# Kernel tuning notes

Measured on AMD Instinct MI355X. Metric: run time of the kernel, lower is better.

## Reference

```python
import math
import jax, jax.numpy as jnp
import numpy as np

B, N = 1, 768
C_S, C_Z, C_H, H, PQ, PV = 384, 128, 16, 12, 4, 8
INF, EPS = 1e5, 1e-8
SOFTPLUS_INV_1 = 0.541324854612918


def setup_inputs() -> dict:
    key = jax.random.key(0)
    ks = jax.random.split(key, 20)
    p = lambda k, shape: (0.02 * jax.random.normal(k, shape)).astype(jnp.float32)
    hc = H * C_H
    inp = {
        's': jax.random.normal(ks[0], (B, N, C_S), dtype=jnp.float32),
        'z': jax.random.normal(ks[1], (B, N, N, C_Z), dtype=jnp.float32),
        'rot': jax.random.normal(ks[2], (B, N, 3, 3), dtype=jnp.float32),
        'trans': jax.random.normal(ks[3], (B, N, 3), dtype=jnp.float32),
        'mask': jnp.ones((B, N), dtype=jnp.float32),
        'w_q': p(ks[4], (hc, C_S)), 'b_q': p(ks[5], (hc,)),
        'w_kv': p(ks[6], (2 * hc, C_S)), 'b_kv': p(ks[7], (2 * hc,)),
        'w_qp': p(ks[8], (H * PQ * 3, C_S)), 'b_qp': p(ks[9], (H * PQ * 3,)),
        'w_kvp': p(ks[10], (H * (PQ + PV) * 3, C_S)), 'b_kvp': p(ks[11], (H * (PQ + PV) * 3,)),
        'w_b': p(ks[12], (H, C_Z)), 'b_b': p(ks[13], (H,)),
        'head_weights': jnp.full((H,), SOFTPLUS_INV_1, dtype=jnp.float32),
        'w_out': p(ks[14], (C_S, H * (C_Z + C_H + PV * 4))), 'b_out': p(ks[15], (C_S,)),
    }
    return inp


def reference(s, z, rot, trans, mask, w_q, b_q, w_kv, b_kv, w_qp, b_qp,
              w_kvp, b_kvp, w_b, b_b, head_weights, w_out, b_out):
    b_, n_ = s.shape[0], s.shape[1]
    # input projections
    q = (s @ w_q.T + b_q).reshape(b_, n_, H, C_H)              # [B,N,H,C]
    kv = (s @ w_kv.T + b_kv).reshape(b_, n_, H, 2 * C_H)
    k, v = kv[..., :C_H], kv[..., C_H:]
    bmat = z @ w_b.T + b_b                                      # [B,N,N,H]

    def make_pts(w, bias, P):
        x = s @ w.T + bias                                      # [B,N,3*H*P]
        # torch: split into 3 chunks of H*P, stack on last dim -> [B,N,H*P,3]
        x = x.reshape(b_, n_, 3, H * P).swapaxes(-1, -2)
        # rigid apply: R x + t (per residue)
        x = jnp.einsum('bnij,bnpj->bnpi', rot, x) + trans[:, :, None, :]
        return x.reshape(b_, n_, H, P, 3)

    q_pts = make_pts(w_qp, b_qp, PQ)                            # [B,N,H,PQ,3]
    kv_pts = make_pts(w_kvp, b_kvp, PQ + PV)
    k_pts, v_pts = kv_pts[..., :PQ, :], kv_pts[..., PQ:, :]     # [B,N,H,PQ/PV,3]

    # scalar QK attention
    a = jnp.einsum('bnhc,bmhc->bhnm', q, k) * math.sqrt(1.0 / (3 * C_H))
    a = a + math.sqrt(1.0 / 3) * jnp.moveaxis(bmat, -1, -3)     # pair bias

    # point-distance attention
    diff = q_pts[:, :, None] - k_pts[:, None]                   # [B,N,M,H,PQ,3]
    pt_att = jnp.sum(diff * diff, axis=-1)                      # [B,N,M,H,PQ]
    hw = jax.nn.softplus(head_weights) * math.sqrt(1.0 / (3 * (PQ * 9.0 / 2)))
    pt_att = -0.5 * jnp.sum(pt_att * hw[:, None], axis=-1)      # [B,N,M,H]
    a = a + jnp.moveaxis(pt_att, -1, -3)                        # [B,H,N,M]

    sq_mask = (mask[:, :, None] * mask[:, None, :] - 1.0) * INF
    a = jax.nn.softmax(a + sq_mask[:, None], axis=-1)           # [B,H,N,M]

    # outputs
    o = jnp.einsum('bhnm,bmhc->bnhc', a, v).reshape(b_, n_, H * C_H)
    o_pt = jnp.einsum('bhnm,bmhpc->bnhpc', a, v_pts)            # [B,N,H,PV,3]
    # rigid invert-apply: R^T (x - t)
    o_pt = jnp.einsum('bnji,bnhpj->bnhpi', rot, o_pt - trans[:, :, None, None, :])
    o_pt_norm = jnp.sqrt(jnp.sum(o_pt ** 2, axis=-1) + EPS).reshape(b_, n_, H * PV)
    o_pt = o_pt.reshape(b_, n_, H * PV, 3)
    o_pair = jnp.einsum('bhnm,bnmc->bnhc', a, z).reshape(b_, n_, H * C_Z)

    o_cat = jnp.concatenate(
        [o, o_pt[..., 0], o_pt[..., 1], o_pt[..., 2], o_pt_norm, o_pair], axis=-1)
    return o_cat @ w_out.T + b_out                              # [B,N,c_s]
```

## Files before the change

### kernel.cpp

```cpp
#include <hip/hip_runtime.h>

#define N_ 768
#define CS 384
#define CZ 128
#define HH 12
#define PQ_ 4
#define PV_ 8

__global__ __launch_bounds__(256, 4) void k_zb(
    const float* __restrict__ z,
    const float* __restrict__ w_b, const float* __restrict__ b_b,
    float* __restrict__ zbT)
{
    const int bid = blockIdx.x;
    const int n  = bid / 12;
    const int m0 = (bid % 12) * 64;
    const int tid = threadIdx.x;

    __shared__ float zs[64 * 133];
    __shared__ float zbt[64 * 13];

    const float4* zsrc = (const float4*)(z + ((size_t)n * N_ + m0) * CZ);
    #pragma unroll
    for (int j = 0; j < 8; ++j) {
        int idx = tid + j * 256;
        float4 zv = zsrc[idx];
        int f  = idx << 2;
        int ml = f >> 7;
        int c  = f & 127;
        float* d = &zs[ml * 133 + c];
        d[0] = zv.x; d[1] = zv.y; d[2] = zv.z; d[3] = zv.w;
    }
    __syncthreads();

    const int ml = tid & 63;
    const int hq = __builtin_amdgcn_readfirstlane(tid >> 6);
    const float* w0 = w_b + (hq * 3 + 0) * CZ;
    const float* w1 = w0 + CZ;
    const float* w2 = w1 + CZ;
    const float* zrow = &zs[ml * 133];
    float a0 = 0.f, a1 = 0.f, a2 = 0.f;
    #pragma unroll 8
    for (int c = 0; c < CZ; ++c) {
        float zv = zrow[c];
        a0 += zv * w0[c];
        a1 += zv * w1[c];
        a2 += zv * w2[c];
    }
    const float s3 = 0.5773502691896258f;
    zbt[ml * 13 + hq * 3 + 0] = s3 * (a0 + b_b[hq * 3 + 0]);
    zbt[ml * 13 + hq * 3 + 1] = s3 * (a1 + b_b[hq * 3 + 1]);
    zbt[ml * 13 + hq * 3 + 2] = s3 * (a2 + b_b[hq * 3 + 2]);
    __syncthreads();

    for (int idx = tid; idx < 768; idx += 256) {
        int h = idx >> 6, mm = idx & 63;
        zbT[(size_t)n * (HH * N_) + h * N_ + m0 + mm] = zbt[mm * 13 + h];
    }
}

__global__ __launch_bounds__(256, 4) void k_proj(
    const float* __restrict__ s,
    const float* __restrict__ rot,
    const float* __restrict__ trans,
    const float* __restrict__ w_q,  const float* __restrict__ b_q,
    const float* __restrict__ w_kv, const float* __restrict__ b_kv,
    const float* __restrict__ w_qp, const float* __restrict__ b_qp,
    const float* __restrict__ w_kvp,const float* __restrict__ b_kvp,
    float* __restrict__ q, float* __restrict__ kT,
    float* __restrict__ qp, float* __restrict__ kpT,
    float* __restrict__ vcat)
{
    const int rt = blockIdx.x % 48;
    const int nt = blockIdx.x / 48;
    const int r0 = rt * 24;
    const int n0 = nt * 64;
    const int tid = threadIdx.x;

    __shared__ float Ws[64][36];
    __shared__ float Ss[64][66];
    __shared__ float Rsh[64][9], Tsh[64][3];
    __shared__ float bsh[24];

    auto vmap = [&](int rv, const float*& wrow, float& bias) {
        if (rv < 192)      { wrow = w_q + (size_t)rv * CS;  bias = b_q[rv]; }
        else if (rv < 576) { int r = rv - 192; wrow = w_kv + (size_t)r * CS; bias = b_kv[r]; }
        else if (rv < 720) { int t = rv - 576; int hp = t / 3, d = t % 3;
                             int r = d * 48 + hp;  wrow = w_qp + (size_t)r * CS;  bias = b_qp[r]; }
        else               { int t = rv - 720; int j = t / 3, d = t % 3;
                             int r = d * 144 + j; wrow = w_kvp + (size_t)r * CS; bias = b_kvp[r]; }
    };

    if (tid < 24) {
        const float* wr; float bb;
        vmap(r0 + tid, wr, bb);
        bsh[tid] = bb;
    }
    if (r0 >= 576) {
        for (int idx = tid; idx < 64 * 9; idx += 256)
            Rsh[idx / 9][idx % 9] = rot[(size_t)(n0 + idx / 9) * 9 + idx % 9];
        for (int idx = tid; idx < 64 * 3; idx += 256)
            Tsh[idx / 3][idx % 3] = trans[(size_t)(n0 + idx / 3) * 3 + idx % 3];
    }

    const int g_n = tid & 31;
    const int g_r = tid >> 5;
    float acc[3][2] = {{0.f,0.f},{0.f,0.f},{0.f,0.f}};

    for (int ks = 0; ks < 6; ++ks) {
        const int kb = ks * 64;
        for (int t4 = tid; t4 < 384; t4 += 256) {
            int rl = t4 >> 4, c4 = t4 & 15;
            const float* wrow; float bb;
            vmap(r0 + rl, wrow, bb);
            float4 wv = *(const float4*)(wrow + kb + c4 * 4);
            int slot = (rl / 3) * 4 + rl % 3;
            Ws[c4 * 4 + 0][slot] = wv.x;
            Ws[c4 * 4 + 1][slot] = wv.y;
            Ws[c4 * 4 + 2][slot] = wv.z;
            Ws[c4 * 4 + 3][slot] = wv.w;
        }
        for (int t4 = tid; t4 < 1024; t4 += 256) {
            int nl = t4 >> 4, c4 = t4 & 15;
            float4 sv = *(const float4*)(s + (size_t)(n0 + nl) * CS + kb + c4 * 4);
            Ss[c4 * 4 + 0][nl] = sv.x;
            Ss[c4 * 4 + 1][nl] = sv.y;
            Ss[c4 * 4 + 2][nl] = sv.z;
            Ss[c4 * 4 + 3][nl] = sv.w;
        }
        __syncthreads();
        #pragma unroll 8
        for (int k = 0; k < 64; ++k) {
            float4 w  = *(const float4*)&Ws[k][g_r * 4];
            float2 sv = *(const float2*)&Ss[k][g_n * 2];
            acc[0][0] += w.x * sv.x;  acc[0][1] += w.x * sv.y;
            acc[1][0] += w.y * sv.x;  acc[1][1] += w.y * sv.y;
            acc[2][0] += w.z * sv.x;  acc[2][1] += w.z * sv.y;
        }
        __syncthreads();
    }

    const float b0 = bsh[g_r * 3 + 0];
    const float b1 = bsh[g_r * 3 + 1];
    const float b2 = bsh[g_r * 3 + 2];
    const int rvb = r0 + g_r * 3;

    if (rvb < 192) {
        #pragma unroll
        for (int nn = 0; nn < 2; ++nn) {
            int n = n0 + g_n * 2 + nn;
            q[(size_t)n * 192 + rvb + 0] = acc[0][nn] + b0;
            q[(size_t)n * 192 + rvb + 1] = acc[1][nn] + b1;
            q[(size_t)n * 192 + rvb + 2] = acc[2][nn] + b2;
        }
    } else if (rvb < 576) {
        #pragma unroll
        for (int cc = 0; cc < 3; ++cc) {
            int i = rvb + cc - 192;
            int h = i >> 5, c = i & 31;
            float bb = (cc == 0) ? b0 : (cc == 1) ? b1 : b2;
            if (c < 16) {
                float2 st = make_float2(acc[cc][0] + bb, acc[cc][1] + bb);
                *(float2*)&kT[(size_t)(h * 16 + c) * N_ + n0 + g_n * 2] = st;
            } else {
                vcat[(size_t)(n0 + g_n * 2 + 0) * 480 + h * 16 + c - 16] = acc[cc][0] + bb;
                vcat[(size_t)(n0 + g_n * 2 + 1) * 480 + h * 16 + c - 16] = acc[cc][1] + bb;
            }
        }
    } else if (rvb < 720) {
        int hp = (rvb - 576) / 3;
        #pragma unroll
        for (int nn = 0; nn < 2; ++nn) {
            int nl = g_n * 2 + nn, n = n0 + nl;
            float x = acc[0][nn] + b0, y = acc[1][nn] + b1, zc = acc[2][nn] + b2;
            const float* R = Rsh[nl];
            const float* T = Tsh[nl];
            #pragma unroll
            for (int d = 0; d < 3; ++d)
                qp[(size_t)n * 144 + hp * 3 + d] =
                    R[d * 3 + 0] * x + R[d * 3 + 1] * y + R[d * 3 + 2] * zc + T[d];
        }
    } else {
        int j = (rvb - 720) / 3;
        int h = j / 12, p = j % 12;
        float px[2][3];
        #pragma unroll
        for (int nn = 0; nn < 2; ++nn) {
            int nl = g_n * 2 + nn;
            float x = acc[0][nn] + b0, y = acc[1][nn] + b1, zc = acc[2][nn] + b2;
            const float* R = Rsh[nl];
            const float* T = Tsh[nl];
            #pragma unroll
            for (int d = 0; d < 3; ++d)
                px[nn][d] = R[d * 3 + 0] * x + R[d * 3 + 1] * y + R[d * 3 + 2] * zc + T[d];
        }
        if (p < PQ_) {
            #pragma unroll
            for (int d = 0; d < 3; ++d)
                *(float2*)&kpT[(size_t)(h * 12 + p * 3 + d) * N_ + n0 + g_n * 2] =
                    make_float2(px[0][d], px[1][d]);
        } else {
            int base = 192 + (h * PV_ + p - PQ_) * 3;
            #pragma unroll
            for (int nn = 0; nn < 2; ++nn) {
                int n = n0 + g_n * 2 + nn;
                #pragma unroll
                for (int d = 0; d < 3; ++d)
                    vcat[(size_t)n * 480 + base + d] = px[nn][d];
            }
        }
    }
}

__global__ __launch_bounds__(256, 4) void k_fused(
    const float* __restrict__ q, const float* __restrict__ kT,
    const float* __restrict__ qp, const float* __restrict__ kpT,
    const float* __restrict__ vcat,
    const float* __restrict__ zbT,
    const float* __restrict__ z,
    const float* __restrict__ head_weights,
    const float* __restrict__ mask,
    const float* __restrict__ rot, const float* __restrict__ trans,
    float* __restrict__ ocat)
{
    const int n   = (N_ - 1) - blockIdx.x;
    const int tid = threadIdx.x;

    __shared__ float qv[192], qpt[144];
    __shared__ float hw[HH];
    __shared__ float L[HH * N_];
    __shared__ float og[288];
    __shared__ float R[9], T[3];

    for (int i = tid; i < 192; i += 256) qv[i] = q[n * 192 + i];
    for (int i = tid; i < 144; i += 256) qpt[i] = qp[n * 144 + i];
    if (tid < HH) {
        float x = head_weights[tid];
        hw[tid] = 0.13608276348795434f * logf(1.0f + expf(x));
    }
    if (tid < 9) R[tid] = rot[n * 9 + tid];
    if (tid < 3) T[tid] = trans[n * 3 + tid];
    __syncthreads();

    const float mn = mask[n];

    if (tid < 192) {
        const int m0 = tid * 4;
        float4 mk = *(const float4*)(mask + m0);
        float mt0 = (mn * mk.x - 1.0f) * 100000.0f;
        float mt1 = (mn * mk.y - 1.0f) * 100000.0f;
        float mt2 = (mn * mk.z - 1.0f) * 100000.0f;
        float mt3 = (mn * mk.w - 1.0f) * 100000.0f;
        const float* zbn = zbT + (size_t)n * (HH * N_);
        #pragma unroll
        for (int h = 0; h < HH; ++h) {
            float ax = 0.f, ay = 0.f, az = 0.f, aw = 0.f;
            #pragma unroll
            for (int c = 0; c < 16; ++c) {
                float qc = qv[h * 16 + c];
                float4 kx = *(const float4*)&kT[(size_t)(h * 16 + c) * N_ + m0];
                ax += qc * kx.x; ay += qc * kx.y; az += qc * kx.z; aw += qc * kx.w;
            }
            const float s48 = 0.14433756729740643f;
            ax *= s48; ay *= s48; az *= s48; aw *= s48;
            float4 zb4 = *(const float4*)&zbn[h * N_ + m0];
            ax += zb4.x; ay += zb4.y; az += zb4.z; aw += zb4.w;
            float dx = 0.f, dy = 0.f, dz = 0.f, dw = 0.f;
            #pragma unroll
            for (int pd = 0; pd < 12; ++pd) {
                float qd = qpt[h * 12 + pd];
                float4 kd = *(const float4*)&kpT[(size_t)(h * 12 + pd) * N_ + m0];
                float ex = qd - kd.x, ey = qd - kd.y, ez = qd - kd.z, ew = qd - kd.w;
                dx += ex * ex; dy += ey * ey; dz += ez * ez; dw += ew * ew;
            }
            float hwh = 0.5f * hw[h];
            float4 out;
            out.x = ax - hwh * dx + mt0;
            out.y = ay - hwh * dy + mt1;
            out.z = az - hwh * dz + mt2;
            out.w = aw - hwh * dw + mt3;
            *(float4*)&L[h * N_ + m0] = out;
        }
    }
    __syncthreads();

    {
        const int wv_ = tid >> 6, lane = tid & 63;
        #pragma unroll
        for (int j = 0; j < 3; ++j) {
            const int h = wv_ + 4 * j;
            float vals[12];
            float mx = -1e30f;
            #pragma unroll
            for (int t = 0; t < 12; ++t) {
                vals[t] = L[h * N_ + lane + 64 * t];
                mx = fmaxf(mx, vals[t]);
            }
            #pragma unroll
            for (int off = 32; off; off >>= 1) mx = fmaxf(mx, __shfl_xor(mx, off));
            float sum = 0.f;
            #pragma unroll
            for (int t = 0; t < 12; ++t) { vals[t] = expf(vals[t] - mx); sum += vals[t]; }
            #pragma unroll
            for (int off = 32; off; off >>= 1) sum += __shfl_xor(sum, off);
            float inv = 1.0f / sum;
            #pragma unroll
            for (int t = 0; t < 12; ++t) L[h * N_ + lane + 64 * t] = vals[t] * inv;
        }
    }
    __syncthreads();

    float* oc = ocat + (size_t)n * 2112;

    {
        const int i0 = tid;
        const int i1 = tid + 256;
        const bool act1 = (i1 < 480);
        const int h0 = (i0 < 192) ? (i0 >> 4) : ((i0 - 192) / 24);
        const int h1 = act1 ? ((i1 - 192) / 24) : 0;
        const float* Lh0 = L + h0 * N_;
        const float* Lh1 = L + h1 * N_;
        const float* vc0 = vcat + i0;
        const float* vc1 = vcat + (act1 ? i1 : 0);
        float a0 = 0.f, a1 = 0.f;
        #pragma unroll 8
        for (int m = 0; m < N_; ++m) {
            float x0 = vc0[(size_t)m * 480];
            float x1 = vc1[(size_t)m * 480];
            a0 += Lh0[m] * x0;
            a1 += Lh1[m] * x1;
        }
        if (i0 < 192) oc[i0] = a0; else og[i0 - 192] = a0;
        if (act1) og[i1 - 192] = a1;
    }

    {
        const int c4 = tid & 31;
        const int g  = tid >> 5;
        const float4* zr = (const float4*)(z + (size_t)n * N_ * CZ) + c4;
        float4 acc[HH];
        #pragma unroll
        for (int h = 0; h < HH; ++h) { acc[h].x = acc[h].y = acc[h].z = acc[h].w = 0.f; }
        const int ms = g * 96;
        #pragma unroll 4
        for (int m = ms; m < ms + 96; ++m) {
            float4 zz = zr[(size_t)m * 32];
            #pragma unroll
            for (int h = 0; h < HH; ++h) {
                float lh = L[h * N_ + m];
                acc[h].x += lh * zz.x; acc[h].y += lh * zz.y;
                acc[h].z += lh * zz.z; acc[h].w += lh * zz.w;
            }
        }
        #pragma unroll
        for (int h = 0; h < HH; ++h) {
            acc[h].x += __shfl_xor(acc[h].x, 32);
            acc[h].y += __shfl_xor(acc[h].y, 32);
            acc[h].z += __shfl_xor(acc[h].z, 32);
            acc[h].w += __shfl_xor(acc[h].w, 32);
        }
        __syncthreads();
        float4* part4 = (float4*)L;
        if ((tid & 63) < 32) {
            const int w = tid >> 6;
            #pragma unroll
            for (int h = 0; h < HH; ++h)
                part4[(w * HH + h) * 32 + c4] = acc[h];
        }
        __syncthreads();
        const float* part = (const float*)L;
        for (int idx = tid; idx < HH * CZ; idx += 256) {
            float sum = part[idx] + part[1536 + idx] + part[3072 + idx] + part[4608 + idx];
            oc[576 + idx] = sum;
        }
    }

    for (int hp = tid; hp < 96; hp += 256) {
        float gx = og[hp * 3 + 0] - T[0];
        float gy = og[hp * 3 + 1] - T[1];
        float gz = og[hp * 3 + 2] - T[2];
        float lx = R[0] * gx + R[3] * gy + R[6] * gz;
        float ly = R[1] * gx + R[4] * gy + R[7] * gz;
        float lz = R[2] * gx + R[5] * gy + R[8] * gz;
        oc[192 + hp] = lx;
        oc[288 + hp] = ly;
        oc[384 + hp] = lz;
        oc[480 + hp] = sqrtf(lx * lx + ly * ly + lz * lz + 1e-8f);
    }
}

__global__ __launch_bounds__(384) void k_init(
    const float* __restrict__ b_out, float* __restrict__ out)
{
    out[(size_t)blockIdx.x * 384 + threadIdx.x] = b_out[threadIdx.x];
}

__global__ __launch_bounds__(256, 6) void k_final(
    const float* __restrict__ ocat,
    const float* __restrict__ w_out,
    float* __restrict__ out)
{
    const int b  = blockIdx.x;
    const int bk = b & 3;
    const int bn = (b >> 2) % 48;
    const int bj = (b >> 2) / 48;
    const int n0 = bn * 16, j0 = bj * 64, kq0 = bk * 528;
    const int tid = threadIdx.x;

    __shared__ float As_t[48][20];
    __shared__ float Bs[64][49];

    const int tj = tid & 63;
    const int tn = tid >> 6;
    float a0 = 0.f, a1 = 0.f, a2 = 0.f, a3 = 0.f;

    for (int st = 0; st < 11; ++st) {
        const int kb = kq0 + st * 48;
        for (int t4 = tid; t4 < 192; t4 += 256) {
            int nl = t4 / 12, c4 = t4 % 12;
            float4 av = *(const float4*)(ocat + (size_t)(n0 + nl) * 2112 + kb + c4 * 4);
            As_t[c4 * 4 + 0][nl] = av.x;
            As_t[c4 * 4 + 1][nl] = av.y;
            As_t[c4 * 4 + 2][nl] = av.z;
            As_t[c4 * 4 + 3][nl] = av.w;
        }
        for (int t4 = tid; t4 < 768; t4 += 256) {
            int jr = t4 / 12, c4 = t4 % 12;
            float4 wv = *(const float4*)(w_out + (size_t)(j0 + jr) * 2112 + kb + c4 * 4);
            Bs[jr][c4 * 4 + 0] = wv.x;
            Bs[jr][c4 * 4 + 1] = wv.y;
            Bs[jr][c4 * 4 + 2] = wv.z;
            Bs[jr][c4 * 4 + 3] = wv.w;
        }
        __syncthreads();
        #pragma unroll 8
        for (int k = 0; k < 48; ++k) {
            float bb = Bs[tj][k];
            float4 av = *(const float4*)&As_t[k][tn * 4];
            a0 += bb * av.x; a1 += bb * av.y; a2 += bb * av.z; a3 += bb * av.w;
        }
        __syncthreads();
    }

    float* op = out + (size_t)(n0 + tn * 4) * 384 + j0 + tj;
    atomicAdd(op + 0 * 384, a0);
    atomicAdd(op + 1 * 384, a1);
    atomicAdd(op + 2 * 384, a2);
    atomicAdd(op + 3 * 384, a3);
}

extern "C" void kernel_launch(void* const* d_in, const int* in_sizes, int n_in,
                              void* d_out, int out_size, void* d_ws, size_t ws_size,
                              hipStream_t stream)
{
    const float* s     = (const float*)d_in[0];
    const float* z     = (const float*)d_in[1];
    const float* rot   = (const float*)d_in[2];
    const float* trans = (const float*)d_in[3];
    const float* mask  = (const float*)d_in[4];
    const float* w_q   = (const float*)d_in[5];
    const float* b_q   = (const float*)d_in[6];
    const float* w_kv  = (const float*)d_in[7];
    const float* b_kv  = (const float*)d_in[8];
    const float* w_qp  = (const float*)d_in[9];
    const float* b_qp  = (const float*)d_in[10];
    const float* w_kvp = (const float*)d_in[11];
    const float* b_kvp = (const float*)d_in[12];
    const float* w_b   = (const float*)d_in[13];
    const float* b_b   = (const float*)d_in[14];
    const float* hwts  = (const float*)d_in[15];
    const float* w_out = (const float*)d_in[16];
    const float* b_out = (const float*)d_in[17];

    float* ws    = (float*)d_ws;
    float* q     = ws;
    float* kT    = q     + 147456;
    float* qp    = kT    + 147456;
    float* kpT   = qp    + 110592;
    float* vcat  = kpT   + 110592;
    float* zbT   = vcat  + 368640;
    float* ocat  = zbT   + 7077888;

    k_init<<<N_, 384, 0, stream>>>(b_out, (float*)d_out);
    k_proj<<<576, 256, 0, stream>>>(s, rot, trans, w_q, b_q, w_kv, b_kv,
                                    w_qp, b_qp, w_kvp, b_kvp, q, kT, qp, kpT, vcat);
    k_zb<<<N_ * 12, 256, 0, stream>>>(z, w_b, b_b, zbT);
    k_fused<<<N_, 256, 0, stream>>>(q, kT, qp, kpT, vcat, zbT, z,
                                    hwts, mask, rot, trans, ocat);
    k_final<<<1152, 256, 0, stream>>>(ocat, w_out, (float*)d_out);
}
```

Measured before the change: 699.3 us.

## Merge front-end kernels and split pair-output reduction into separate high-parallelism kernel

Fuses the bias-init, projection and z-bias kernels into one launch, branching on block index. The o_pair reduction over z moves out of the per-row attention kernel into a new kernel that splits each row's M dimension six ways and combines partial sums with atomicAdd. The attention kernel now writes its softmax probabilities back into the zbT buffer, and the new kernel reads them from there. This aims to spread the large z read across many more blocks than the 768 per-row blocks allowed. It costs an extra global round trip for the probabilities, zero-initialisation of the outputs and atomic contention.

```diff
diff --git a/kernel.cpp b/kernel.cpp
--- a/kernel.cpp
+++ b/kernel.cpp
@@ -7,59 +7,7 @@
 #define PQ_ 4
 #define PV_ 8
 
-__global__ __launch_bounds__(256, 4) void k_zb(
-    const float* __restrict__ z,
-    const float* __restrict__ w_b, const float* __restrict__ b_b,
-    float* __restrict__ zbT)
-{
-    const int bid = blockIdx.x;
-    const int n  = bid / 12;
-    const int m0 = (bid % 12) * 64;
-    const int tid = threadIdx.x;
-
-    __shared__ float zs[64 * 133];
-    __shared__ float zbt[64 * 13];
-
-    const float4* zsrc = (const float4*)(z + ((size_t)n * N_ + m0) * CZ);
-    #pragma unroll
-    for (int j = 0; j < 8; ++j) {
-        int idx = tid + j * 256;
-        float4 zv = zsrc[idx];
-        int f  = idx << 2;
-        int ml = f >> 7;
-        int c  = f & 127;
-        float* d = &zs[ml * 133 + c];
-        d[0] = zv.x; d[1] = zv.y; d[2] = zv.z; d[3] = zv.w;
-    }
-    __syncthreads();
-
-    const int ml = tid & 63;
-    const int hq = __builtin_amdgcn_readfirstlane(tid >> 6);
-    const float* w0 = w_b + (hq * 3 + 0) * CZ;
-    const float* w1 = w0 + CZ;
-    const float* w2 = w1 + CZ;
-    const float* zrow = &zs[ml * 133];
-    float a0 = 0.f, a1 = 0.f, a2 = 0.f;
-    #pragma unroll 8
-    for (int c = 0; c < CZ; ++c) {
-        float zv = zrow[c];
-        a0 += zv * w0[c];
-        a1 += zv * w1[c];
-        a2 += zv * w2[c];
-    }
-    const float s3 = 0.5773502691896258f;
-    zbt[ml * 13 + hq * 3 + 0] = s3 * (a0 + b_b[hq * 3 + 0]);
-    zbt[ml * 13 + hq * 3 + 1] = s3 * (a1 + b_b[hq * 3 + 1]);
-    zbt[ml * 13 + hq * 3 + 2] = s3 * (a2 + b_b[hq * 3 + 2]);
-    __syncthreads();
-
-    for (int idx = tid; idx < 768; idx += 256) {
-        int h = idx >> 6, mm = idx & 63;
-        zbT[(size_t)n * (HH * N_) + h * N_ + m0 + mm] = zbt[mm * 13 + h];
-    }
-}
-
-__global__ __launch_bounds__(256, 4) void k_proj(
+__global__ __launch_bounds__(256, 4) void k_front(
     const float* __restrict__ s,
     const float* __restrict__ rot,
     const float* __restrict__ trans,
@@ -67,148 +15,206 @@
     const float* __restrict__ w_kv, const float* __restrict__ b_kv,
     const float* __restrict__ w_qp, const float* __restrict__ b_qp,
     const float* __restrict__ w_kvp,const float* __restrict__ b_kvp,
+    const float* __restrict__ z,
+    const float* __restrict__ w_b, const float* __restrict__ b_b,
+    const float* __restrict__ b_out,
     float* __restrict__ q, float* __restrict__ kT,
     float* __restrict__ qp, float* __restrict__ kpT,
-    float* __restrict__ vcat)
+    float* __restrict__ vcat,
+    float* __restrict__ zbT,
+    float* __restrict__ out)
 {
-    const int rt = blockIdx.x % 48;
-    const int nt = blockIdx.x / 48;
-    const int r0 = rt * 24;
-    const int n0 = nt * 64;
+    __shared__ __align__(16) float smem[9344];
+    const int bid = blockIdx.x;
     const int tid = threadIdx.x;
 
-    __shared__ float Ws[64][36];
-    __shared__ float Ss[64][66];
-    __shared__ float Rsh[64][9], Tsh[64][3];
-    __shared__ float bsh[24];
-
-    auto vmap = [&](int rv, const float*& wrow, float& bias) {
-        if (rv < 192)      { wrow = w_q + (size_t)rv * CS;  bias = b_q[rv]; }
-        else if (rv < 576) { int r = rv - 192; wrow = w_kv + (size_t)r * CS; bias = b_kv[r]; }
-        else if (rv < 720) { int t = rv - 576; int hp = t / 3, d = t % 3;
-                             int r = d * 48 + hp;  wrow = w_qp + (size_t)r * CS;  bias = b_qp[r]; }
-        else               { int t = rv - 720; int j = t / 3, d = t % 3;
-                             int r = d * 144 + j; wrow = w_kvp + (size_t)r * CS; bias = b_kvp[r]; }
-    };
-
-    if (tid < 24) {
-        const float* wr; float bb;
-        vmap(r0 + tid, wr, bb);
-        bsh[tid] = bb;
-    }
-    if (r0 >= 576) {
-        for (int idx = tid; idx < 64 * 9; idx += 256)
-            Rsh[idx / 9][idx % 9] = rot[(size_t)(n0 + idx / 9) * 9 + idx % 9];
-        for (int idx = tid; idx < 64 * 3; idx += 256)
-            Tsh[idx / 3][idx % 3] = trans[(size_t)(n0 + idx / 3) * 3 + idx % 3];
-    }
-
-    const int g_n = tid & 31;
-    const int g_r = tid >> 5;
-    float acc[3][2] = {{0.f,0.f},{0.f,0.f},{0.f,0.f}};
-
-    for (int ks = 0; ks < 6; ++ks) {
-        const int kb = ks * 64;
-        for (int t4 = tid; t4 < 384; t4 += 256) {
-            int rl = t4 >> 4, c4 = t4 & 15;
-            const float* wrow; float bb;
-            vmap(r0 + rl, wrow, bb);
-            float4 wv = *(const float4*)(wrow + kb + c4 * 4);
-            int slot = (rl / 3) * 4 + rl % 3;
-            Ws[c4 * 4 + 0][slot] = wv.x;
-            Ws[c4 * 4 + 1][slot] = wv.y;
-            Ws[c4 * 4 + 2][slot] = wv.z;
-            Ws[c4 * 4 + 3][slot] = wv.w;
-        }
-        for (int t4 = tid; t4 < 1024; t4 += 256) {
-            int nl = t4 >> 4, c4 = t4 & 15;
-            float4 sv = *(const float4*)(s + (size_t)(n0 + nl) * CS + kb + c4 * 4);
-            Ss[c4 * 4 + 0][nl] = sv.x;
-            Ss[c4 * 4 + 1][nl] = sv.y;
-            Ss[c4 * 4 + 2][nl] = sv.z;
-            Ss[c4 * 4 + 3][nl] = sv.w;
+    if (bid < 9216) {
+        float* zs  = smem;
+        float* zbt = smem + 8512;
+        const int n  = bid / 12;
+        const int m0 = (bid % 12) * 64;
+
+        const float4* zsrc = (const float4*)(z + ((size_t)n * N_ + m0) * CZ);
+        #pragma unroll
+        for (int j = 0; j < 8; ++j) {
+            int idx = tid + j * 256;
+            float4 zv = zsrc[idx];
+            int f  = idx << 2;
+            int ml = f >> 7;
+            int c  = f & 127;
+            float* d = &zs[ml * 133 + c];
+            d[0] = zv.x; d[1] = zv.y; d[2] = zv.z; d[3] = zv.w;
         }
         __syncthreads();
+
+        const int ml = tid & 63;
+        const int hq = __builtin_amdgcn_readfirstlane(tid >> 6);
+        const float* w0 = w_b + (hq * 3 + 0) * CZ;
+        const float* w1 = w0 + CZ;
+        const float* w2 = w1 + CZ;
+        const float* zrow = &zs[ml * 133];
+        float a0 = 0.f, a1 = 0.f, a2 = 0.f;
         #pragma unroll 8
-        for (int k = 0; k < 64; ++k) {
-            float4 w  = *(const float4*)&Ws[k][g_r * 4];
-            float2 sv = *(const float2*)&Ss[k][g_n * 2];
-            acc[0][0] += w.x * sv.x;  acc[0][1] += w.x * sv.y;
-            acc[1][0] += w.y * sv.x;  acc[1][1] += w.y * sv.y;
-            acc[2][0] += w.z * sv.x;  acc[2][1] += w.z * sv.y;
-        }
+        for (int c = 0; c < CZ; ++c) {
+            float zv = zrow[c];
+            a0 += zv * w0[c];
+            a1 += zv * w1[c];
+            a2 += zv * w2[c];
+        }
+        const float s3 = 0.5773502691896258f;
+        zbt[ml * 13 + hq * 3 + 0] = s3 * (a0 + b_b[hq * 3 + 0]);
+        zbt[ml * 13 + hq * 3 + 1] = s3 * (a1 + b_b[hq * 3 + 1]);
+        zbt[ml * 13 + hq * 3 + 2] = s3 * (a2 + b_b[hq * 3 + 2]);
         __syncthreads();
-    }
-
-    const float b0 = bsh[g_r * 3 + 0];
-    const float b1 = bsh[g_r * 3 + 1];
-    const float b2 = bsh[g_r * 3 + 2];
-    const int rvb = r0 + g_r * 3;
-
-    if (rvb < 192) {
-        #pragma unroll
-        for (int nn = 0; nn < 2; ++nn) {
-            int n = n0 + g_n * 2 + nn;
-            q[(size_t)n * 192 + rvb + 0] = acc[0][nn] + b0;
-            q[(size_t)n * 192 + rvb + 1] = acc[1][nn] + b1;
-            q[(size_t)n * 192 + rvb + 2] = acc[2][nn] + b2;
-        }
-    } else if (rvb < 576) {
-        #pragma unroll
-        for (int cc = 0; cc < 3; ++cc) {
-            int i = rvb + cc - 192;
-            int h = i >> 5, c = i & 31;
-            float bb = (cc == 0) ? b0 : (cc == 1) ? b1 : b2;
-            if (c < 16) {
-                float2 st = make_float2(acc[cc][0] + bb, acc[cc][1] + bb);
-                *(float2*)&kT[(size_t)(h * 16 + c) * N_ + n0 + g_n * 2] = st;
-            } else {
-                vcat[(size_t)(n0 + g_n * 2 + 0) * 480 + h * 16 + c - 16] = acc[cc][0] + bb;
-                vcat[(size_t)(n0 + g_n * 2 + 1) * 480 + h * 16 + c - 16] = acc[cc][1] + bb;
-            }
-        }
-    } else if (rvb < 720) {
-        int hp = (rvb - 576) / 3;
-        #pragma unroll
-        for (int nn = 0; nn < 2; ++nn) {
-            int nl = g_n * 2 + nn, n = n0 + nl;
-            float x = acc[0][nn] + b0, y = acc[1][nn] + b1, zc = acc[2][nn] + b2;
-            const float* R = Rsh[nl];
-            const float* T = Tsh[nl];
-            #pragma unroll
-            for (int d = 0; d < 3; ++d)
-                qp[(size_t)n * 144 + hp * 3 + d] =
-                    R[d * 3 + 0] * x + R[d * 3 + 1] * y + R[d * 3 + 2] * zc + T[d];
-        }
-    } else {
-        int j = (rvb - 720) / 3;
-        int h = j / 12, p = j % 12;
-        float px[2][3];
-        #pragma unroll
-        for (int nn = 0; nn < 2; ++nn) {
-            int nl = g_n * 2 + nn;
-            float x = acc[0][nn] + b0, y = acc[1][nn] + b1, zc = acc[2][nn] + b2;
-            const float* R = Rsh[nl];
-            const float* T = Tsh[nl];
-            #pragma unroll
-            for (int d = 0; d < 3; ++d)
-                px[nn][d] = R[d * 3 + 0] * x + R[d * 3 + 1] * y + R[d * 3 + 2] * zc + T[d];
-        }
-        if (p < PQ_) {
-            #pragma unroll
-            for (int d = 0; d < 3; ++d)
-                *(float2*)&kpT[(size_t)(h * 12 + p * 3 + d) * N_ + n0 + g_n * 2] =
-                    make_float2(px[0][d], px[1][d]);
-        } else {
-            int base = 192 + (h * PV_ + p - PQ_) * 3;
+
+        for (int idx = tid; idx < 768; idx += 256) {
+            int h = idx >> 6, mm = idx & 63;
+            zbT[(size_t)n * (HH * N_) + h * N_ + m0 + mm] = zbt[mm * 13 + h];
+        }
+    } else if (bid < 9792) {
+        const int b2 = bid - 9216;
+        const int rt = b2 % 48;
+        const int nt = b2 / 48;
+        const int r0 = rt * 24;
+        const int n0 = nt * 64;
+
+        float (*Ws)[36] = (float(*)[36])smem;
+        float (*Ss)[66] = (float(*)[66])(smem + 2304);
+        float (*Rsh)[9] = (float(*)[9])(smem + 6528);
+        float (*Tsh)[3] = (float(*)[3])(smem + 7104);
+        float* bsh      = smem + 7296;
+
+        auto vmap = [&](int rv, const float*& wrow, float& bias) {
+            if (rv < 192)      { wrow = w_q + (size_t)rv * CS;  bias = b_q[rv]; }
+            else if (rv < 576) { int r = rv - 192; wrow = w_kv + (size_t)r * CS; bias = b_kv[r]; }
+            else if (rv < 720) { int t = rv - 576; int hp = t / 3, d = t % 3;
+                                 int r = d * 48 + hp;  wrow = w_qp + (size_t)r * CS;  bias = b_qp[r]; }
+            else               { int t = rv - 720; int j = t / 3, d = t % 3;
+                                 int r = d * 144 + j; wrow = w_kvp + (size_t)r * CS; bias = b_kvp[r]; }
+        };
+
+        if (tid < 24) {
+            const float* wr; float bb;
+            vmap(r0 + tid, wr, bb);
+            bsh[tid] = bb;
+        }
+        if (r0 >= 576) {
+            for (int idx = tid; idx < 64 * 9; idx += 256)
+                Rsh[idx / 9][idx % 9] = rot[(size_t)(n0 + idx / 9) * 9 + idx % 9];
+            for (int idx = tid; idx < 64 * 3; idx += 256)
+                Tsh[idx / 3][idx % 3] = trans[(size_t)(n0 + idx / 3) * 3 + idx % 3];
+        }
+
+        const int g_n = tid & 31;
+        const int g_r = tid >> 5;
+        float acc[3][2] = {{0.f,0.f},{0.f,0.f},{0.f,0.f}};
+
+        for (int ks = 0; ks < 6; ++ks) {
+            const int kb = ks * 64;
+            for (int t4 = tid; t4 < 384; t4 += 256) {
+                int rl = t4 >> 4, c4 = t4 & 15;
+                const float* wrow; float bb;
+                vmap(r0 + rl, wrow, bb);
+                float4 wv = *(const float4*)(wrow + kb + c4 * 4);
+                int slot = (rl / 3) * 4 + rl % 3;
+                Ws[c4 * 4 + 0][slot] = wv.x;
+                Ws[c4 * 4 + 1][slot] = wv.y;
+                Ws[c4 * 4 + 2][slot] = wv.z;
+                Ws[c4 * 4 + 3][slot] = wv.w;
+            }
+            for (int t4 = tid; t4 < 1024; t4 += 256) {
+                int nl = t4 >> 4, c4 = t4 & 15;
+                float4 sv = *(const float4*)(s + (size_t)(n0 + nl) * CS + kb + c4 * 4);
+                Ss[c4 * 4 + 0][nl] = sv.x;
+                Ss[c4 * 4 + 1][nl] = sv.y;
+                Ss[c4 * 4 + 2][nl] = sv.z;
+                Ss[c4 * 4 + 3][nl] = sv.w;
+            }
+            __syncthreads();
+            #pragma unroll 8
+            for (int k = 0; k < 64; ++k) {
+                float4 w  = *(const float4*)&Ws[k][g_r * 4];
+                float2 sv = *(const float2*)&Ss[k][g_n * 2];
+                acc[0][0] += w.x * sv.x;  acc[0][1] += w.x * sv.y;
+                acc[1][0] += w.y * sv.x;  acc[1][1] += w.y * sv.y;
+                acc[2][0] += w.z * sv.x;  acc[2][1] += w.z * sv.y;
+            }
+            __syncthreads();
+        }
+
+        const float b0 = bsh[g_r * 3 + 0];
+        const float b1 = bsh[g_r * 3 + 1];
+        const float b2v = bsh[g_r * 3 + 2];
+        const int rvb = r0 + g_r * 3;
+
+        if (rvb < 192) {
             #pragma unroll
             for (int nn = 0; nn < 2; ++nn) {
                 int n = n0 + g_n * 2 + nn;
+                q[(size_t)n * 192 + rvb + 0] = acc[0][nn] + b0;
+                q[(size_t)n * 192 + rvb + 1] = acc[1][nn] + b1;
+                q[(size_t)n * 192 + rvb + 2] = acc[2][nn] + b2v;
+            }
+        } else if (rvb < 576) {
+            #pragma unroll
+            for (int cc = 0; cc < 3; ++cc) {
+                int i = rvb + cc - 192;
+                int h = i >> 5, c = i & 31;
+                float bb = (cc == 0) ? b0 : (cc == 1) ? b1 : b2v;
+                if (c < 16) {
+                    float2 st = make_float2(acc[cc][0] + bb, acc[cc][1] + bb);
+                    *(float2*)&kT[(size_t)(h * 16 + c) * N_ + n0 + g_n * 2] = st;
+                } else {
+                    vcat[(size_t)(n0 + g_n * 2 + 0) * 480 + h * 16 + c - 16] = acc[cc][0] + bb;
+                    vcat[(size_t)(n0 + g_n * 2 + 1) * 480 + h * 16 + c - 16] = acc[cc][1] + bb;
+                }
+            }
+        } else if (rvb < 720) {
+            int hp = (rvb - 576) / 3;
+            #pragma unroll
+            for (int nn = 0; nn < 2; ++nn) {
+                int nl = g_n * 2 + nn, n = n0 + nl;
+                float x = acc[0][nn] + b0, y = acc[1][nn] + b1, zc = acc[2][nn] + b2v;
+                const float* R = Rsh[nl];
+                const float* T = Tsh[nl];
                 #pragma unroll
                 for (int d = 0; d < 3; ++d)
-                    vcat[(size_t)n * 480 + base + d] = px[nn][d];
-            }
-        }
+                    qp[(size_t)n * 144 + hp * 3 + d] =
+                        R[d * 3 + 0] * x + R[d * 3 + 1] * y + R[d * 3 + 2] * zc + T[d];
+            }
+        } else {
+            int j = (rvb - 720) / 3;
+            int h = j / 12, p = j % 12;
+            float px[2][3];
+            #pragma unroll
+            for (int nn = 0; nn < 2; ++nn) {
+                int nl = g_n * 2 + nn;
+                float x = acc[0][nn] + b0, y = acc[1][nn] + b1, zc = acc[2][nn] + b2v;
+                const float* R = Rsh[nl];
+                const float* T = Tsh[nl];
+                #pragma unroll
+                for (int d = 0; d < 3; ++d)
+                    px[nn][d] = R[d * 3 + 0] * x + R[d * 3 + 1] * y + R[d * 3 + 2] * zc + T[d];
+            }
+            if (p < PQ_) {
+                #pragma unroll
+                for (int d = 0; d < 3; ++d)
+                    *(float2*)&kpT[(size_t)(h * 12 + p * 3 + d) * N_ + n0 + g_n * 2] =
+                        make_float2(px[0][d], px[1][d]);
+            } else {
+                int base = 192 + (h * PV_ + p - PQ_) * 3;
+                #pragma unroll
+                for (int nn = 0; nn < 2; ++nn) {
+                    int n = n0 + g_n * 2 + nn;
+                    #pragma unroll
+                    for (int d = 0; d < 3; ++d)
+                        vcat[(size_t)n * 480 + base + d] = px[nn][d];
+                }
+            }
+        }
+    } else {
+        const int idx = (bid - 9792) * 256 + tid;
+        out[idx] = b_out[idx % 384];
     }
 }
 
@@ -216,8 +222,7 @@
     const float* __restrict__ q, const float* __restrict__ kT,
     const float* __restrict__ qp, const float* __restrict__ kpT,
     const float* __restrict__ vcat,
-    const float* __restrict__ zbT,
-    const float* __restrict__ z,
+    float* __restrict__ zbT,
     const float* __restrict__ head_weights,
     const float* __restrict__ mask,
     const float* __restrict__ rot, const float* __restrict__ trans,
@@ -228,7 +233,7 @@
 
     __shared__ float qv[192], qpt[144];
     __shared__ float hw[HH];
-    __shared__ float L[HH * N_];
+    __shared__ __align__(16) float L[HH * N_];
     __shared__ float og[288];
     __shared__ float R[9], T[3];
 
@@ -311,6 +316,13 @@
     __syncthreads();
 
     float* oc = ocat + (size_t)n * 2112;
+
+    {
+        float4* dst = (float4*)(zbT + (size_t)n * (HH * N_));
+        const float4* src = (const float4*)L;
+        for (int i4 = tid; i4 < HH * N_ / 4; i4 += 256) dst[i4] = src[i4];
+    }
+    for (int i = tid; i < HH * CZ; i += 256) oc[576 + i] = 0.f;
 
     {
         const int i0 = tid;
@@ -333,47 +345,7 @@
         if (i0 < 192) oc[i0] = a0; else og[i0 - 192] = a0;
         if (act1) og[i1 - 192] = a1;
     }
-
-    {
-        const int c4 = tid & 31;
-        const int g  = tid >> 5;
-        const float4* zr = (const float4*)(z + (size_t)n * N_ * CZ) + c4;
-        float4 acc[HH];
-        #pragma unroll
-        for (int h = 0; h < HH; ++h) { acc[h].x = acc[h].y = acc[h].z = acc[h].w = 0.f; }
-        const int ms = g * 96;
-        #pragma unroll 4
-        for (int m = ms; m < ms + 96; ++m) {
-            float4 zz = zr[(size_t)m * 32];
-            #pragma unroll
-            for (int h = 0; h < HH; ++h) {
-                float lh = L[h * N_ + m];
-                acc[h].x += lh * zz.x; acc[h].y += lh * zz.y;
-                acc[h].z += lh * zz.z; acc[h].w += lh * zz.w;
-            }
-        }
-        #pragma unroll
-        for (int h = 0; h < HH; ++h) {
-            acc[h].x += __shfl_xor(acc[h].x, 32);
-            acc[h].y += __shfl_xor(acc[h].y, 32);
-            acc[h].z += __shfl_xor(acc[h].z, 32);
-            acc[h].w += __shfl_xor(acc[h].w, 32);
-        }
-        __syncthreads();
-        float4* part4 = (float4*)L;
-        if ((tid & 63) < 32) {
-            const int w = tid >> 6;
-            #pragma unroll
-            for (int h = 0; h < HH; ++h)
-                part4[(w * HH + h) * 32 + c4] = acc[h];
-        }
-        __syncthreads();
-        const float* part = (const float*)L;
-        for (int idx = tid; idx < HH * CZ; idx += 256) {
-            float sum = part[idx] + part[1536 + idx] + part[3072 + idx] + part[4608 + idx];
-            oc[576 + idx] = sum;
-        }
-    }
+    __syncthreads();
 
     for (int hp = tid; hp < 96; hp += 256) {
         float gx = og[hp * 3 + 0] - T[0];
@@ -389,10 +361,63 @@
     }
 }
 
-__global__ __launch_bounds__(384) void k_init(
-    const float* __restrict__ b_out, float* __restrict__ out)
+__global__ __launch_bounds__(256, 5) void k_opair(
+    const float* __restrict__ probs,
+    const float* __restrict__ z,
+    float* __restrict__ ocat)
 {
-    out[(size_t)blockIdx.x * 384 + threadIdx.x] = b_out[threadIdx.x];
+    const int bid = blockIdx.x;
+    const int n   = (N_ - 1) - (bid / 6);
+    const int mt  = bid % 6;
+    const int tid = threadIdx.x;
+
+    __shared__ float Ls[HH][128];
+    __shared__ float4 part[4][HH][32];
+
+    const float* Lr = probs + (size_t)n * (HH * N_);
+    for (int i = tid; i < HH * 128; i += 256)
+        Ls[i >> 7][i & 127] = Lr[(i >> 7) * N_ + mt * 128 + (i & 127)];
+    __syncthreads();
+
+    const int c4 = tid & 31, g = tid >> 5;
+    float4 acc[HH];
+    #pragma unroll
+    for (int h = 0; h < HH; ++h) { acc[h].x = acc[h].y = acc[h].z = acc[h].w = 0.f; }
+
+    const float4* zr = (const float4*)(z + (size_t)n * N_ * CZ) + c4;
+    const int ms = mt * 128 + g * 16;
+    #pragma unroll 4
+    for (int mm = 0; mm < 16; ++mm) {
+        float4 zz = zr[(size_t)(ms + mm) * 32];
+        const int ml = g * 16 + mm;
+        #pragma unroll
+        for (int h = 0; h < HH; ++h) {
+            float lh = Ls[h][ml];
+            acc[h].x += lh * zz.x; acc[h].y += lh * zz.y;
+            acc[h].z += lh * zz.z; acc[h].w += lh * zz.w;
+        }
+    }
+    #pragma unroll
+    for (int h = 0; h < HH; ++h) {
+        acc[h].x += __shfl_xor(acc[h].x, 32);
+        acc[h].y += __shfl_xor(acc[h].y, 32);
+        acc[h].z += __shfl_xor(acc[h].z, 32);
+        acc[h].w += __shfl_xor(acc[h].w, 32);
+    }
+    if ((tid & 63) < 32) {
+        const int w = tid >> 6;
+        #pragma unroll
+        for (int h = 0; h < HH; ++h) part[w][h][c4] = acc[h];
+    }
+    __syncthreads();
+
+    float* oc = ocat + (size_t)n * 2112 + 576;
+    const float* p0 = (const float*)part[0];
+    const float* p1 = (const float*)part[1];
+    const float* p2 = (const float*)part[2];
+    const float* p3 = (const float*)part[3];
+    for (int i = tid; i < HH * CZ; i += 256)
+        atomicAdd(&oc[i], p0[i] + p1[i] + p2[i] + p3[i]);
 }
 
 __global__ __launch_bounds__(256, 6) void k_final(
@@ -481,11 +506,12 @@
     float* zbT   = vcat  + 368640;
     float* ocat  = zbT   + 7077888;
 
-    k_init<<<N_, 384, 0, stream>>>(b_out, (float*)d_out);
-    k_proj<<<576, 256, 0, stream>>>(s, rot, trans, w_q, b_q, w_kv, b_kv,
-                                    w_qp, b_qp, w_kvp, b_kvp, q, kT, qp, kpT, vcat);
-    k_zb<<<N_ * 12, 256, 0, stream>>>(z, w_b, b_b, zbT);
-    k_fused<<<N_, 256, 0, stream>>>(q, kT, qp, kpT, vcat, zbT, z,
+    k_front<<<10944, 256, 0, stream>>>(s, rot, trans, w_q, b_q, w_kv, b_kv,
+                                       w_qp, b_qp, w_kvp, b_kvp, z, w_b, b_b,
+                                       b_out, q, kT, qp, kpT, vcat, zbT,
+                                       (float*)d_out);
+    k_fused<<<N_, 256, 0, stream>>>(q, kT, qp, kpT, vcat, zbT,
                                     hwts, mask, rot, trans, ocat);
+    k_opair<<<N_ * 6, 256, 0, stream>>>(zbT, z, ocat);
     k_final<<<1152, 256, 0, stream>>>(ocat, w_out, (float*)d_out);
 }
```

Result: slower. 816.5 us (+16.8%).
